# Kernel optimization log

Hardware: AMD Instinct MI355X
Metric: run time of the kernel (lower is better)

Reference implementation:

```python
import jax, jax.numpy as jnp
import numpy as np


def _squash(x, eps=1e-8):
    # squash along last (feature) dim: v = s * ||s||^2 / (1+||s||^2) / ||s||
    n2 = jnp.sum(x * x, axis=-1, keepdims=True)
    return x * (n2 / (1.0 + n2)) / jnp.sqrt(n2 + eps)


def setup_inputs() -> dict:
    key = jax.random.key(0)
    k1, k2 = jax.random.split(key)
    B, N_IN, N_CAPS, N_FEAT = 16, 2048, 64, 16
    inputs = jax.random.normal(k1, (B, N_IN, N_CAPS, N_FEAT), dtype=jnp.float32)
    bias = jax.random.normal(k2, (N_CAPS, N_FEAT), dtype=jnp.float32) * 0.02
    return {"inputs": inputs, "bias": bias, "num_routing": 3}


def reference(inputs, bias, num_routing):
    # inputs: [B, n_in, n_caps, n_feat]; bias: [n_caps, n_feat]
    priors = jnp.zeros_like(inputs)
    outputs = None
    for i in range(num_routing):
        agreements = jax.nn.softmax(priors, axis=-2)            # over n_caps
        outputs = jnp.sum(inputs * agreements, axis=-3, keepdims=True)  # [B,1,n_caps,n_feat]
        outputs = _squash(outputs + bias)
        if i < num_routing - 1:
            priors = priors + jnp.sum(inputs * outputs, axis=-1, keepdims=True)
    return outputs[:, 0]  # [B, n_caps, n_feat]
```

## Files before the change

kernel.cpp:

```cpp
#include <hip/hip_runtime.h>
#include <hip/hip_fp16.h>
#include <math.h>

#define BB 16
#define NIN 2048
#define NC 64
#define NF 16
#define BLOCKS_PER_B 64
#define NPBLK (BB * BLOCKS_PER_B)

__device__ __forceinline__ float dot4(float4 a, float4 b) {
    return a.x * b.x + a.y * b.y + a.z * b.z + a.w * b.w;
}

__device__ __forceinline__ unsigned pack2(float x, float y) {
    __half2 h = __float22half2_rn(make_float2(x, y));
    return *reinterpret_cast<unsigned*>(&h);
}

__device__ __forceinline__ float2 unpack2(unsigned u) {
    __half2 h = *reinterpret_cast<__half2*>(&u);
    return __half22float2(h);
}

__device__ __forceinline__ float4 unpack4(unsigned a, unsigned b) {
    float2 f0 = unpack2(a), f1 = unpack2(b);
    return make_float4(f0.x, f0.y, f1.x, f1.y);
}

__global__ __launch_bounds__(256) void pass_mean(const float* __restrict__ in,
                                                 uint2* __restrict__ part2,
                                                 uint4* __restrict__ cp) {
    const int b = blockIdx.x >> 6;
    const int blk = blockIdx.x & 63;
    const int lane = threadIdx.x & 63;
    const int wave = threadIdx.x >> 6;

    const float4* in4 = (const float4*)in;

    float4 acc[4];
#pragma unroll
    for (int k = 0; k < 4; ++k) acc[k] = make_float4(0.f, 0.f, 0.f, 0.f);

#pragma unroll
    for (int t = 0; t < 8; ++t) {
        const size_t i = (size_t)b * NIN + blk * 32 + wave * 8 + t;
        const size_t row = i * 256;
#pragma unroll
        for (int k = 0; k < 2; ++k) {
            float4 v0 = in4[row + 2 * (lane + 64 * k)];
            float4 v1 = in4[row + 2 * (lane + 64 * k) + 1];
            acc[2 * k].x += v0.x; acc[2 * k].y += v0.y;
            acc[2 * k].z += v0.z; acc[2 * k].w += v0.w;
            acc[2 * k + 1].x += v1.x; acc[2 * k + 1].y += v1.y;
            acc[2 * k + 1].z += v1.z; acc[2 * k + 1].w += v1.w;
            uint4 u;
            u.x = pack2(v0.x, v0.y); u.y = pack2(v0.z, v0.w);
            u.z = pack2(v1.x, v1.y); u.w = pack2(v1.z, v1.w);
            cp[i * 128 + lane + 64 * k] = u;
        }
    }

    __shared__ float4 red[4 * 256];
    const int s0a = 2 * lane, s0b = 2 * lane + 128;
    red[wave * 256 + s0a] = acc[0];
    red[wave * 256 + s0a + 1] = acc[1];
    red[wave * 256 + s0b] = acc[2];
    red[wave * 256 + s0b + 1] = acc[3];
    __syncthreads();

    const int t = threadIdx.x;
    float4 s = red[t];
#pragma unroll
    for (int w = 1; w < 4; ++w) {
        float4 r = red[w * 256 + t];
        s.x += r.x; s.y += r.y; s.z += r.z; s.w += r.w;
    }
    uint2 o;
    o.x = pack2(s.x, s.y);
    o.y = pack2(s.z, s.w);
    part2[blockIdx.x * 256 + t] = o;
}

__global__ __launch_bounds__(256) void pass_route(const uint4* __restrict__ cp,
                                                  const float* __restrict__ wv,
                                                  uint2* __restrict__ part2) {
    const int b = blockIdx.x >> 6;
    const int blk = blockIdx.x & 63;
    const int lane = threadIdx.x & 63;
    const int wave = threadIdx.x >> 6;
    const float4* wv4 = (const float4*)wv + (size_t)b * 256;

    float4 ow[4];
    ow[0] = wv4[2 * lane];
    ow[1] = wv4[2 * lane + 1];
    ow[2] = wv4[2 * lane + 128];
    ow[3] = wv4[2 * lane + 129];

    float4 acc[4];
#pragma unroll
    for (int k = 0; k < 4; ++k) acc[k] = make_float4(0.f, 0.f, 0.f, 0.f);

#pragma unroll
    for (int t = 0; t < 8; ++t) {
        const size_t i = (size_t)b * NIN + blk * 32 + wave * 8 + t;
        const uint4 u0 = cp[i * 128 + lane];
        const uint4 u1 = cp[i * 128 + lane + 64];
        float4 v00 = unpack4(u0.x, u0.y), v01 = unpack4(u0.z, u0.w);
        float4 v10 = unpack4(u1.x, u1.y), v11 = unpack4(u1.z, u1.w);

        float d0 = dot4(v00, ow[0]) + dot4(v01, ow[1]);
        float d1 = dot4(v10, ow[2]) + dot4(v11, ow[3]);
        d0 += __shfl_xor(d0, 1);
        d1 += __shfl_xor(d1, 1);

        float m = fmaxf(d0, d1);
        m = fmaxf(m, __shfl_xor(m, 2));
        m = fmaxf(m, __shfl_xor(m, 4));
        m = fmaxf(m, __shfl_xor(m, 8));
        m = fmaxf(m, __shfl_xor(m, 16));
        m = fmaxf(m, __shfl_xor(m, 32));
        float e0 = __expf(d0 - m), e1 = __expf(d1 - m);
        float ss = e0 + e1;
        ss += __shfl_xor(ss, 2);
        ss += __shfl_xor(ss, 4);
        ss += __shfl_xor(ss, 8);
        ss += __shfl_xor(ss, 16);
        ss += __shfl_xor(ss, 32);
        const float inv = 1.0f / ss;
        const float a0 = e0 * inv, a1 = e1 * inv;
        acc[0].x += a0 * v00.x; acc[0].y += a0 * v00.y;
        acc[0].z += a0 * v00.z; acc[0].w += a0 * v00.w;
        acc[1].x += a0 * v01.x; acc[1].y += a0 * v01.y;
        acc[1].z += a0 * v01.z; acc[1].w += a0 * v01.w;
        acc[2].x += a1 * v10.x; acc[2].y += a1 * v10.y;
        acc[2].z += a1 * v10.z; acc[2].w += a1 * v10.w;
        acc[3].x += a1 * v11.x; acc[3].y += a1 * v11.y;
        acc[3].z += a1 * v11.z; acc[3].w += a1 * v11.w;
    }

    __shared__ float4 red[4 * 256];
    const int s0a = 2 * lane, s0b = 2 * lane + 128;
    red[wave * 256 + s0a] = acc[0];
    red[wave * 256 + s0a + 1] = acc[1];
    red[wave * 256 + s0b] = acc[2];
    red[wave * 256 + s0b + 1] = acc[3];
    __syncthreads();

    const int t = threadIdx.x;
    float4 s = red[t];
#pragma unroll
    for (int w = 1; w < 4; ++w) {
        float4 r = red[w * 256 + t];
        s.x += r.x; s.y += r.y; s.z += r.z; s.w += r.w;
    }
    uint2 o;
    o.x = pack2(s.x, s.y);
    o.y = pack2(s.z, s.w);
    part2[blockIdx.x * 256 + t] = o;
}

__global__ __launch_bounds__(256) void reduce_squash(const uint2* __restrict__ part2,
                                                     const float* __restrict__ bias,
                                                     const float* __restrict__ prev,
                                                     float* __restrict__ dst,
                                                     float scale) {
    const int b = blockIdx.x >> 6;
    const int c = blockIdx.x & 63;
    const int tid = threadIdx.x;
    const int q = tid >> 2;
    const int h4 = tid & 3;

    const uint2 u = part2[(size_t)(b * BLOCKS_PER_B + q) * 256 + c * 4 + h4];
    const float4 f = unpack4(u.x, u.y);

    __shared__ float lds[1024];
    lds[q * 16 + h4 * 4 + 0] = f.x;
    lds[q * 16 + h4 * 4 + 1] = f.y;
    lds[q * 16 + h4 * 4 + 2] = f.z;
    lds[q * 16 + h4 * 4 + 3] = f.w;
    __syncthreads();

    __shared__ float red[256];
    {
        const int f16 = tid & 15;
        const int qg = tid >> 4;
        float s = 0.f;
#pragma unroll
        for (int j = 0; j < 4; ++j) s += lds[(qg * 4 + j) * 16 + f16];
        red[tid] = s;
    }
    __syncthreads();
    if (tid < 128) red[tid] += red[tid + 128];
    __syncthreads();
    if (tid < 64) red[tid] += red[tid + 64];
    __syncthreads();
    if (tid < 32) red[tid] += red[tid + 32];
    __syncthreads();
    if (tid < 16) {
        float s = (red[tid] + red[tid + 16]) * scale + bias[c * NF + tid];
        float n2 = s * s;
        n2 += __shfl_xor(n2, 1);
        n2 += __shfl_xor(n2, 2);
        n2 += __shfl_xor(n2, 4);
        n2 += __shfl_xor(n2, 8);
        const float sc = n2 / (1.0f + n2) / sqrtf(n2 + 1e-8f);
        float o = s * sc;
        const size_t oi = (size_t)b * 1024 + c * NF + tid;
        if (prev) o += prev[oi];
        dst[oi] = o;
    }
}

extern "C" void kernel_launch(void* const* d_in, const int* in_sizes, int n_in,
                              void* d_out, int out_size, void* d_ws, size_t ws_size,
                              hipStream_t stream) {
    const float* in = (const float*)d_in[0];
    const float* bias = (const float*)d_in[1];

    float* ws = (float*)d_ws;
    uint2* part2 = (uint2*)ws;
    float* out0 = ws + (size_t)NPBLK * 512;
    float* osum = out0 + 16384;
    uint4* cp = (uint4*)(osum + 16384);

    dim3 grid(NPBLK), blk(256);
    pass_mean<<<grid, blk, 0, stream>>>(in, part2, cp);
    reduce_squash<<<1024, 256, 0, stream>>>(part2, bias, nullptr, out0, 1.0f / 64.0f);
    pass_route<<<grid, blk, 0, stream>>>(cp, out0, part2);
    reduce_squash<<<1024, 256, 0, stream>>>(part2, bias, out0, osum, 1.0f);
    pass_route<<<grid, blk, 0, stream>>>(cp, osum, part2);
    reduce_squash<<<1024, 256, 0, stream>>>(part2, bias, nullptr, (float*)d_out, 1.0f);
}
```

Measured before the change: 85.90 us.

## Fuse partial reduction and squash into routing pass prologue

Removes the two intermediate reduce_squash launches by having each routing block re-reduce the 64 partial sums for its batch, apply bias and squash, and optionally add the previous output, all in its prologue. Block 0 of each batch writes the squashed weights for the next iteration. This cuts two kernel launches and their serialization. In exchange, every block redundantly reads 64×256 partials, which adds global and L2 traffic.

```diff
diff --git a/kernel.cpp b/kernel.cpp
--- a/kernel.cpp
+++ b/kernel.cpp
@@ -4,8 +4,6 @@
 
 #define BB 16
 #define NIN 2048
-#define NC 64
-#define NF 16
 #define BLOCKS_PER_B 64
 #define NPBLK (BB * BLOCKS_PER_B)
 
@@ -18,14 +16,12 @@
     return *reinterpret_cast<unsigned*>(&h);
 }
 
-__device__ __forceinline__ float2 unpack2(unsigned u) {
-    __half2 h = *reinterpret_cast<__half2*>(&u);
-    return __half22float2(h);
-}
-
 __device__ __forceinline__ float4 unpack4(unsigned a, unsigned b) {
-    float2 f0 = unpack2(a), f1 = unpack2(b);
-    return make_float4(f0.x, f0.y, f1.x, f1.y);
+    __half2 ha = *reinterpret_cast<__half2*>(&a);
+    __half2 hb = *reinterpret_cast<__half2*>(&b);
+    float2 fa = __half22float2(ha);
+    float2 fb = __half22float2(hb);
+    return make_float4(fa.x, fa.y, fb.x, fb.y);
 }
 
 __global__ __launch_bounds__(256) void pass_mean(const float* __restrict__ in,
@@ -76,31 +72,56 @@
         float4 r = red[w * 256 + t];
         s.x += r.x; s.y += r.y; s.z += r.z; s.w += r.w;
     }
-    uint2 o;
-    o.x = pack2(s.x, s.y);
-    o.y = pack2(s.z, s.w);
-    part2[blockIdx.x * 256 + t] = o;
-}
-
-__global__ __launch_bounds__(256) void pass_route(const uint4* __restrict__ cp,
-                                                  const float* __restrict__ wv,
-                                                  uint2* __restrict__ part2) {
-    const int b = blockIdx.x >> 6;
-    const int blk = blockIdx.x & 63;
-    const int lane = threadIdx.x & 63;
-    const int wave = threadIdx.x >> 6;
-    const float4* wv4 = (const float4*)wv + (size_t)b * 256;
-
-    float4 ow[4];
-    ow[0] = wv4[2 * lane];
-    ow[1] = wv4[2 * lane + 1];
-    ow[2] = wv4[2 * lane + 128];
-    ow[3] = wv4[2 * lane + 129];
-
-    float4 acc[4];
-#pragma unroll
-    for (int k = 0; k < 4; ++k) acc[k] = make_float4(0.f, 0.f, 0.f, 0.f);
-
+    part2[(size_t)blockIdx.x * 256 + t] = make_uint2(pack2(s.x, s.y), pack2(s.z, s.w));
+}
+
+__global__ __launch_bounds__(256) void pass_route_f(const uint4* __restrict__ cp,
+                                                    const uint2* __restrict__ partIn,
+                                                    const float* __restrict__ bias,
+                                                    const float4* __restrict__ prevW,
+                                                    float scale,
+                                                    uint2* __restrict__ partOut,
+                                                    float4* __restrict__ outW) {
+    const int bid = blockIdx.x;
+    const int b = bid >> 6;
+    const int blk = bid & 63;
+    const int tid = threadIdx.x;
+    const int lane = tid & 63;
+    const int wave = tid >> 6;
+
+    __shared__ float4 wls[256];
+    __shared__ float4 red[4 * 256];
+
+    float4 rs = make_float4(0.f, 0.f, 0.f, 0.f);
+#pragma unroll 8
+    for (int q = 0; q < 64; ++q) {
+        uint2 u = partIn[(size_t)((b << 6) + q) * 256 + tid];
+        float4 f = unpack4(u.x, u.y);
+        rs.x += f.x; rs.y += f.y; rs.z += f.z; rs.w += f.w;
+    }
+    const float4 bv = ((const float4*)bias)[tid];
+    float4 s4 = make_float4(rs.x * scale + bv.x, rs.y * scale + bv.y,
+                            rs.z * scale + bv.z, rs.w * scale + bv.w);
+    float n2 = dot4(s4, s4);
+    n2 += __shfl_xor(n2, 1);
+    n2 += __shfl_xor(n2, 2);
+    const float sc = n2 / (1.0f + n2) / sqrtf(n2 + 1e-8f);
+    float4 w4 = make_float4(s4.x * sc, s4.y * sc, s4.z * sc, s4.w * sc);
+    if (prevW) {
+        const float4 p = prevW[(size_t)b * 256 + tid];
+        w4.x += p.x; w4.y += p.y; w4.z += p.z; w4.w += p.w;
+    }
+    if (outW && blk == 0) outW[(size_t)b * 256 + tid] = w4;
+    wls[tid] = w4;
+    __syncthreads();
+
+    const float4 ow0 = wls[2 * lane];
+    const float4 ow1 = wls[2 * lane + 1];
+    const float4 ow2 = wls[2 * lane + 128];
+    const float4 ow3 = wls[2 * lane + 129];
+
+    float4 r0 = make_float4(0.f, 0.f, 0.f, 0.f);
+    float4 r1 = r0, r2 = r0, r3 = r0;
 #pragma unroll
     for (int t = 0; t < 8; ++t) {
         const size_t i = (size_t)b * NIN + blk * 32 + wave * 8 + t;
@@ -109,8 +130,8 @@
         float4 v00 = unpack4(u0.x, u0.y), v01 = unpack4(u0.z, u0.w);
         float4 v10 = unpack4(u1.x, u1.y), v11 = unpack4(u1.z, u1.w);
 
-        float d0 = dot4(v00, ow[0]) + dot4(v01, ow[1]);
-        float d1 = dot4(v10, ow[2]) + dot4(v11, ow[3]);
+        float d0 = dot4(v00, ow0) + dot4(v01, ow1);
+        float d1 = dot4(v10, ow2) + dot4(v11, ow3);
         d0 += __shfl_xor(d0, 1);
         d1 += __shfl_xor(d1, 1);
 
@@ -129,42 +150,35 @@
         ss += __shfl_xor(ss, 32);
         const float inv = 1.0f / ss;
         const float a0 = e0 * inv, a1 = e1 * inv;
-        acc[0].x += a0 * v00.x; acc[0].y += a0 * v00.y;
-        acc[0].z += a0 * v00.z; acc[0].w += a0 * v00.w;
-        acc[1].x += a0 * v01.x; acc[1].y += a0 * v01.y;
-        acc[1].z += a0 * v01.z; acc[1].w += a0 * v01.w;
-        acc[2].x += a1 * v10.x; acc[2].y += a1 * v10.y;
-        acc[2].z += a1 * v10.z; acc[2].w += a1 * v10.w;
-        acc[3].x += a1 * v11.x; acc[3].y += a1 * v11.y;
-        acc[3].z += a1 * v11.z; acc[3].w += a1 * v11.w;
-    }
-
-    __shared__ float4 red[4 * 256];
+        r0.x += a0 * v00.x; r0.y += a0 * v00.y;
+        r0.z += a0 * v00.z; r0.w += a0 * v00.w;
+        r1.x += a0 * v01.x; r1.y += a0 * v01.y;
+        r1.z += a0 * v01.z; r1.w += a0 * v01.w;
+        r2.x += a1 * v10.x; r2.y += a1 * v10.y;
+        r2.z += a1 * v10.z; r2.w += a1 * v10.w;
+        r3.x += a1 * v11.x; r3.y += a1 * v11.y;
+        r3.z += a1 * v11.z; r3.w += a1 * v11.w;
+    }
+
     const int s0a = 2 * lane, s0b = 2 * lane + 128;
-    red[wave * 256 + s0a] = acc[0];
-    red[wave * 256 + s0a + 1] = acc[1];
-    red[wave * 256 + s0b] = acc[2];
-    red[wave * 256 + s0b + 1] = acc[3];
-    __syncthreads();
-
-    const int t = threadIdx.x;
-    float4 s = red[t];
+    red[wave * 256 + s0a] = r0;
+    red[wave * 256 + s0a + 1] = r1;
+    red[wave * 256 + s0b] = r2;
+    red[wave * 256 + s0b + 1] = r3;
+    __syncthreads();
+
+    float4 s = red[tid];
 #pragma unroll
     for (int w = 1; w < 4; ++w) {
-        float4 r = red[w * 256 + t];
+        float4 r = red[w * 256 + tid];
         s.x += r.x; s.y += r.y; s.z += r.z; s.w += r.w;
     }
-    uint2 o;
-    o.x = pack2(s.x, s.y);
-    o.y = pack2(s.z, s.w);
-    part2[blockIdx.x * 256 + t] = o;
+    partOut[(size_t)bid * 256 + tid] = make_uint2(pack2(s.x, s.y), pack2(s.z, s.w));
 }
 
 __global__ __launch_bounds__(256) void reduce_squash(const uint2* __restrict__ part2,
                                                      const float* __restrict__ bias,
-                                                     const float* __restrict__ prev,
-                                                     float* __restrict__ dst,
-                                                     float scale) {
+                                                     float* __restrict__ dst) {
     const int b = blockIdx.x >> 6;
     const int c = blockIdx.x & 63;
     const int tid = threadIdx.x;
@@ -198,17 +212,14 @@
     if (tid < 32) red[tid] += red[tid + 32];
     __syncthreads();
     if (tid < 16) {
-        float s = (red[tid] + red[tid + 16]) * scale + bias[c * NF + tid];
+        float s = red[tid] + red[tid + 16] + bias[c * 16 + tid];
         float n2 = s * s;
         n2 += __shfl_xor(n2, 1);
         n2 += __shfl_xor(n2, 2);
         n2 += __shfl_xor(n2, 4);
         n2 += __shfl_xor(n2, 8);
         const float sc = n2 / (1.0f + n2) / sqrtf(n2 + 1e-8f);
-        float o = s * sc;
-        const size_t oi = (size_t)b * 1024 + c * NF + tid;
-        if (prev) o += prev[oi];
-        dst[oi] = o;
+        dst[(size_t)b * 1024 + c * 16 + tid] = s * sc;
     }
 }
 
@@ -218,17 +229,18 @@
     const float* in = (const float*)d_in[0];
     const float* bias = (const float*)d_in[1];
 
-    float* ws = (float*)d_ws;
-    uint2* part2 = (uint2*)ws;
-    float* out0 = ws + (size_t)NPBLK * 512;
-    float* osum = out0 + 16384;
-    uint4* cp = (uint4*)(osum + 16384);
+    char* ws = (char*)d_ws;
+    uint2* part0 = (uint2*)ws;
+    uint2* part1 = (uint2*)(ws + (2 << 20));
+    uint2* part2 = (uint2*)(ws + (4 << 20));
+    float4* out0b = (float4*)(ws + (6 << 20));
+    uint4* cp = (uint4*)(ws + (7 << 20));
 
     dim3 grid(NPBLK), blk(256);
-    pass_mean<<<grid, blk, 0, stream>>>(in, part2, cp);
-    reduce_squash<<<1024, 256, 0, stream>>>(part2, bias, nullptr, out0, 1.0f / 64.0f);
-    pass_route<<<grid, blk, 0, stream>>>(cp, out0, part2);
-    reduce_squash<<<1024, 256, 0, stream>>>(part2, bias, out0, osum, 1.0f);
-    pass_route<<<grid, blk, 0, stream>>>(cp, osum, part2);
-    reduce_squash<<<1024, 256, 0, stream>>>(part2, bias, nullptr, (float*)d_out, 1.0f);
-}
+    pass_mean<<<grid, blk, 0, stream>>>(in, part0, cp);
+    pass_route_f<<<grid, blk, 0, stream>>>(cp, part0, bias, nullptr,
+                                           1.0f / 64.0f, part1, out0b);
+    pass_route_f<<<grid, blk, 0, stream>>>(cp, part1, bias, out0b,
+                                           1.0f, part2, nullptr);
+    reduce_squash<<<grid, blk, 0, stream>>>(part2, bias, (float*)d_out);
+}
```

Measured after the change: 92.55 us. +7.7%, slower.
